# Kernel tuning notes

Hardware: AMD Instinct MI355X
Metric: run time of the kernel (lower is better)

## Reference

```python
import jax, jax.numpy as jnp
import numpy as np

S_MIN = 0.01
S_MAX = 36500.0
SEQ_LEN = 128
BATCH = 65536


def setup_inputs() -> dict:
    key = jax.random.key(0)
    k1, k2 = jax.random.split(key)
    # elapsed days: nonnegative floats; ratings: integers 1..4 stored as float
    t = jax.random.uniform(k1, (SEQ_LEN, BATCH), dtype=jnp.float32) * 30.0
    rating = jax.random.randint(k2, (SEQ_LEN, BATCH), 1, 5).astype(jnp.float32)
    inputs = jnp.stack([t, rating], axis=-1)  # [S, B, 2]
    w = jnp.array([0.4, 0.6, 2.4, 5.8, 4.93, 0.94, 0.86, 0.01, 1.49,
                   0.14, 0.94, 2.18, 0.05, 0.34, 1.26, 0.29, 2.61],
                  dtype=jnp.float32)
    return {"inputs": inputs, "w": w}


def _first_step(X, w):
    # state is all-zeros only on the first step (clamp keeps s >= S_MIN after)
    rating = X[:, 1]
    ridx = jnp.clip(rating.astype(jnp.int32) - 1, 0, 3)
    valid = (rating >= 1) & (rating <= 4)
    new_s = jnp.where(valid, w[ridx], 1.0)
    new_d = jnp.clip(w[4] - w[5] * (rating - 3.0), 1.0, 10.0)
    new_s = jnp.clip(new_s, S_MIN, S_MAX)
    return jnp.stack([new_s, new_d], axis=1)  # [B, 2]


def _step(w, state, X):
    s, d = state[:, 0], state[:, 1]
    t, rating = X[:, 0], X[:, 1]
    # power forgetting curve: r = (1 + t / (9 s))^-1
    r = 1.0 / (1.0 + t / (9.0 * s))
    hard_penalty = jnp.where(rating == 2, w[15], 1.0)
    easy_bonus = jnp.where(rating == 4, w[16], 1.0)
    s_success = s * (1.0 + jnp.exp(w[8]) * (11.0 - d) * jnp.power(s, -w[9])
                     * (jnp.exp((1.0 - r) * w[10]) - 1.0)
                     * hard_penalty * easy_bonus)
    s_failure = jnp.minimum(
        w[11] * jnp.power(d, -w[12]) * (jnp.power(s + 1.0, w[13]) - 1.0)
        * jnp.exp((1.0 - r) * w[14]),
        s)
    new_s = jnp.where(rating > 1.0, s_success, s_failure)
    new_d = d - w[6] * (rating - 3.0)
    new_d = w[7] * w[4] + (1.0 - w[7]) * new_d  # mean reversion to w[4]
    new_d = jnp.clip(new_d, 1.0, 10.0)
    new_s = jnp.clip(new_s, S_MIN, S_MAX)
    new_state = jnp.stack([new_s, new_d], axis=1)
    return new_state, new_state


def reference(inputs, w):
    state0 = _first_step(inputs[0], w)  # [B, 2]
    final_state, rest = jax.lax.scan(lambda st, X: _step(w, st, X),
                                     state0, inputs[1:])
    outputs = jnp.concatenate([state0[None], rest], axis=0)  # [S, B, 2]
    return outputs, final_state
```

## Files before the change

### kernel.cpp

```cpp
#include <hip/hip_runtime.h>

#define BATCH_N 65536
#define SEQ_N   128
#define DEPTH   16

typedef float v2f __attribute__((ext_vector_type(2)));

__global__ __launch_bounds__(256) void fsrs_kernel(
    const v2f* __restrict__ in,
    const float* __restrict__ w,
    v2f*       __restrict__ out)
{
    const int b = blockIdx.x * 256 + threadIdx.x;

    const float w0 = w[0], w1 = w[1], w2 = w[2], w3 = w[3];
    const float w4 = w[4], w5 = w[5], w6 = w[6], w7 = w[7];
    const float w9 = w[9], w11 = w[11], w12 = w[12], w13 = w[13];
    const float w15 = w[15], w16 = w[16];
    constexpr float LOG2E = 1.44269504088896340736f;
    const float w8l  = w[8]  * LOG2E;
    const float w10l = w[10] * LOG2E;
    const float w14l = w[14] * LOG2E;
    const float omw7   = 1.0f - w7;
    const float omw7w6 = omw7 * w6;
    const float dc0    = w7 * w4 + 3.0f * omw7w6;

    const v2f* ip = in  + b;
    v2f*       op = out + b;

    float s = 0.01f, d = 1.0f;

    auto step = [&](v2f x) {
        const float tt     = x.x;
        const float rating = x.y;
        const float nineS = 9.0f * s;
        const float rc  = __builtin_amdgcn_rcpf(nineS + tt);
        const float omr = tt * rc;
        const float hb = (rating == 2.0f) ? w15 : ((rating == 4.0f) ? w16 : 1.0f);

        const float log2s = __builtin_amdgcn_logf(s);
        const float ex    = __builtin_amdgcn_exp2f(__builtin_fmaf(-w9, log2s, w8l));
        const float e10   = __builtin_amdgcn_exp2f(omr * w10l);
        const float su    = ex * (11.0f - d) * (e10 - 1.0f) * hb;
        const float s_succ = __builtin_fmaf(su, s, s);

        const float log2d  = __builtin_amdgcn_logf(d);
        const float powd   = __builtin_amdgcn_exp2f(-w12 * log2d);
        const float log2s1 = __builtin_amdgcn_logf(s + 1.0f);
        const float pows1  = __builtin_amdgcn_exp2f(w13 * log2s1);
        const float e14    = __builtin_amdgcn_exp2f(omr * w14l);
        const float s_fail = fminf(w11 * powd * (pows1 - 1.0f) * e14, s);

        const float ns = (rating > 1.0f) ? s_succ : s_fail;
        const float nd = __builtin_fmaf(omw7, d, __builtin_fmaf(-omw7w6, rating, dc0));
        d = fminf(fmaxf(nd, 1.0f), 10.0f);
        s = fminf(fmaxf(ns, 0.01f), 36500.0f);
    };

    auto st = [&](int row) {
        v2f o; o.x = s; o.y = d;
        __builtin_nontemporal_store(o, &op[row * BATCH_N]);
    };

    v2f A[DEPTH], B[DEPTH];

#pragma unroll
    for (int i = 0; i < DEPTH; ++i) A[i] = ip[i * BATCH_N];

#pragma unroll
    for (int i = 0; i < DEPTH; ++i) B[i] = ip[(DEPTH + i) * BATCH_N];
    {
        const float rating = A[0].y;
        const float wsel = (rating < 2.5f) ? ((rating < 1.5f) ? w0 : w1)
                                           : ((rating < 3.5f) ? w2 : w3);
        const float ns = (rating >= 1.0f && rating <= 4.0f) ? wsel : 1.0f;
        const float nd = w4 - w5 * (rating - 3.0f);
        d = fminf(fmaxf(nd, 1.0f), 10.0f);
        s = fminf(fmaxf(ns, 0.01f), 36500.0f);
        st(0);
    }
#pragma unroll
    for (int i = 1; i < DEPTH; ++i) { step(A[i]); st(i); }

#pragma unroll 1
    for (int c = 0; c < 3; ++c) {
        const int ra = 32 + c * 32;
#pragma unroll
        for (int i = 0; i < DEPTH; ++i) A[i] = ip[(ra + i) * BATCH_N];
#pragma unroll
        for (int i = 0; i < DEPTH; ++i) { step(B[i]); st(ra - DEPTH + i); }
#pragma unroll
        for (int i = 0; i < DEPTH; ++i) B[i] = ip[(ra + DEPTH + i) * BATCH_N];
#pragma unroll
        for (int i = 0; i < DEPTH; ++i) { step(A[i]); st(ra + i); }
    }

#pragma unroll
    for (int i = 0; i < DEPTH; ++i) { step(B[i]); st(112 + i); }

    {
        v2f o; o.x = s; o.y = d;
        op[SEQ_N * BATCH_N] = o;
    }
}

extern "C" void kernel_launch(void* const* d_in, const int* in_sizes, int n_in,
                              void* d_out, int out_size, void* d_ws, size_t ws_size,
                              hipStream_t stream) {
    const v2f*   in = (const v2f*)d_in[0];
    const float* w  = (const float*)d_in[1];
    v2f* out = (v2f*)d_out;
    fsrs_kernel<<<BATCH_N / 256, 256, 0, stream>>>(in, w, out);
}
```

Baseline: 116.0 us.

## Precompute difficulty chain per chunk and merge success/failure transcendental paths

The difficulty recurrence does not depend on stability, so it is now computed ahead for each 16-step chunk, along with its pow term and the hard/easy multiplier, and packed into a signed per-step coefficient. The serial stability step then picks one branch by sign and evaluates a single exp2 for the retention term and a single exp2 for the power term, instead of computing both the success and failure expressions. This shortens the dependent chain and cuts transcendental work per step, at the cost of three extra 16-entry register arrays per buffer, which raises register pressure.

```diff
diff --git a/kernel.cpp b/kernel.cpp
--- a/kernel.cpp
+++ b/kernel.cpp
@@ -2,7 +2,6 @@
 
 #define BATCH_N 65536
 #define SEQ_N   128
-#define DEPTH   16
 
 typedef float v2f __attribute__((ext_vector_type(2)));
 
@@ -28,78 +27,101 @@
     const v2f* ip = in  + b;
     v2f*       op = out + b;
 
-    float s = 0.01f, d = 1.0f;
+    float s = 0.01f;
+    float dcur = 1.0f;
+    float dpre = 1.0f;
 
-    auto step = [&](v2f x) {
-        const float tt     = x.x;
-        const float rating = x.y;
-        const float nineS = 9.0f * s;
-        const float rc  = __builtin_amdgcn_rcpf(nineS + tt);
-        const float omr = tt * rc;
-        const float hb = (rating == 2.0f) ? w15 : ((rating == 4.0f) ? w16 : 1.0f);
+    v2f rawA[16], rawB[16];
+    float tA[16], dA[16], mA[16];
+    float tB[16], dB[16], mB[16];
 
-        const float log2s = __builtin_amdgcn_logf(s);
-        const float ex    = __builtin_amdgcn_exp2f(__builtin_fmaf(-w9, log2s, w8l));
-        const float e10   = __builtin_amdgcn_exp2f(omr * w10l);
-        const float su    = ex * (11.0f - d) * (e10 - 1.0f) * hb;
-        const float s_succ = __builtin_fmaf(su, s, s);
-
-        const float log2d  = __builtin_amdgcn_logf(d);
-        const float powd   = __builtin_amdgcn_exp2f(-w12 * log2d);
-        const float log2s1 = __builtin_amdgcn_logf(s + 1.0f);
-        const float pows1  = __builtin_amdgcn_exp2f(w13 * log2s1);
-        const float e14    = __builtin_amdgcn_exp2f(omr * w14l);
-        const float s_fail = fminf(w11 * powd * (pows1 - 1.0f) * e14, s);
-
-        const float ns = (rating > 1.0f) ? s_succ : s_fail;
-        const float nd = __builtin_fmaf(omw7, d, __builtin_fmaf(-omw7w6, rating, dc0));
-        d = fminf(fmaxf(nd, 1.0f), 10.0f);
-        s = fminf(fmaxf(ns, 0.01f), 36500.0f);
+    auto loadC = [&](v2f* raw, int base) {
+#pragma unroll
+        for (int i = 0; i < 16; ++i) raw[i] = ip[(base + i) * BATCH_N];
     };
 
-    auto st = [&](int row) {
-        v2f o; o.x = s; o.y = d;
-        __builtin_nontemporal_store(o, &op[row * BATCH_N]);
+    auto preC = [&](const v2f* raw, float* T, float* D, float* M, int lo) {
+#pragma unroll
+        for (int i = 0; i < 16; ++i) {
+            if (i < lo) continue;
+            const float tt = raw[i].x, rating = raw[i].y;
+            const float hb = (rating == 2.0f) ? w15
+                           : ((rating == 4.0f) ? w16 : 1.0f);
+            const float eh = (11.0f - dpre) * hb;
+            const float m2 = w11 * __builtin_amdgcn_exp2f(
+                                 -w12 * __builtin_amdgcn_logf(dpre));
+            M[i] = (rating > 1.0f) ? eh : -m2;
+            const float nd = __builtin_fmaf(omw7, dpre,
+                              __builtin_fmaf(-omw7w6, rating, dc0));
+            dpre = fminf(fmaxf(nd, 1.0f), 10.0f);
+            T[i] = tt;
+            D[i] = dpre;
+        }
     };
 
-    v2f A[DEPTH], B[DEPTH];
+    auto stepC = [&](const float* T, const float* D, const float* M,
+                     int base, int lo) {
+#pragma unroll
+        for (int i = 0; i < 16; ++i) {
+            if (i < lo) continue;
+            const float tt = T[i], ms = M[i];
+            const bool  sel = ms > 0.0f;
+            const float q   = __builtin_fmaf(9.0f, s, tt);
+            const float omr = tt * __builtin_amdgcn_rcpf(q);
+            const float e   = __builtin_amdgcn_exp2f(omr * (sel ? w10l : w14l));
+            const float a1  = __builtin_fmaf(-w9, __builtin_amdgcn_logf(s), w8l);
+            const float a2  = w13 * __builtin_amdgcn_logf(s + 1.0f);
+            const float A   = __builtin_amdgcn_exp2f(sel ? a1 : a2);
+            const float Af  = sel ? A          : (A - 1.0f);
+            const float Ef  = sel ? (e - 1.0f) : e;
+            const float m   = sel ? (ms * s)   : (-ms);
+            const float P   = Af * Ef * m;
+            const float ns  = sel ? (s + P) : fminf(P, s);
+            s = fminf(fmaxf(ns, 0.01f), 36500.0f);
+            dcur = D[i];
+            v2f o; o.x = s; o.y = dcur;
+            __builtin_nontemporal_store(o, &op[(base + i) * BATCH_N]);
+        }
+    };
 
-#pragma unroll
-    for (int i = 0; i < DEPTH; ++i) A[i] = ip[i * BATCH_N];
+    loadC(rawA, 0);
+    {
+        const float rating = rawA[0].y;
+        const float d0 = fminf(fmaxf(w4 - w5 * (rating - 3.0f), 1.0f), 10.0f);
+        dpre = d0;
+        tA[0] = rawA[0].x; dA[0] = d0; mA[0] = 1.0f;
+    }
+    preC(rawA, tA, dA, mA, 1);
 
-#pragma unroll
-    for (int i = 0; i < DEPTH; ++i) B[i] = ip[(DEPTH + i) * BATCH_N];
+    loadC(rawB, 16);
     {
-        const float rating = A[0].y;
+        const float rating = rawA[0].y;
         const float wsel = (rating < 2.5f) ? ((rating < 1.5f) ? w0 : w1)
                                            : ((rating < 3.5f) ? w2 : w3);
         const float ns = (rating >= 1.0f && rating <= 4.0f) ? wsel : 1.0f;
-        const float nd = w4 - w5 * (rating - 3.0f);
-        d = fminf(fmaxf(nd, 1.0f), 10.0f);
         s = fminf(fmaxf(ns, 0.01f), 36500.0f);
-        st(0);
+        dcur = dA[0];
+        v2f o; o.x = s; o.y = dcur;
+        __builtin_nontemporal_store(o, &op[0]);
     }
-#pragma unroll
-    for (int i = 1; i < DEPTH; ++i) { step(A[i]); st(i); }
+    stepC(tA, dA, mA, 0, 1);
+    preC(rawB, tB, dB, mB, 0);
 
 #pragma unroll 1
     for (int c = 0; c < 3; ++c) {
-        const int ra = 32 + c * 32;
-#pragma unroll
-        for (int i = 0; i < DEPTH; ++i) A[i] = ip[(ra + i) * BATCH_N];
-#pragma unroll
-        for (int i = 0; i < DEPTH; ++i) { step(B[i]); st(ra - DEPTH + i); }
-#pragma unroll
-        for (int i = 0; i < DEPTH; ++i) B[i] = ip[(ra + DEPTH + i) * BATCH_N];
-#pragma unroll
-        for (int i = 0; i < DEPTH; ++i) { step(A[i]); st(ra + i); }
+        loadC(rawA, 32 * c + 32);
+        stepC(tB, dB, mB, 32 * c + 16, 0);
+        preC(rawA, tA, dA, mA, 0);
+
+        loadC(rawB, 32 * c + 48);
+        stepC(tA, dA, mA, 32 * c + 32, 0);
+        preC(rawB, tB, dB, mB, 0);
     }
 
-#pragma unroll
-    for (int i = 0; i < DEPTH; ++i) { step(B[i]); st(112 + i); }
+    stepC(tB, dB, mB, 112, 0);
 
     {
-        v2f o; o.x = s; o.y = d;
+        v2f o; o.x = s; o.y = dcur;
         op[SEQ_N * BATCH_N] = o;
     }
 }
```

Result: no change. 114.9 us (-1.0%).
